# Performance work log

Hardware: AMD Instinct MI355X
Metric: run time of the kernel (lower is better)

Reference implementation:

```python
import jax, jax.numpy as jnp
import numpy as np

N_USERS = 100_000
N_ITEMS = 50_000
N = N_USERS + N_ITEMS
N_LAYERS = 3
ALPHA = 0.8
D = 64
IMG_D = 4096
TXT_D = 384
N_INTER = 2_000_000  # user-item interactions; symmetric nnz = 2*N_INTER


def setup_inputs() -> dict:
    # --- build symmetric-normalized bipartite adjacency (D^-1/2 A D^-1/2) in numpy ---
    rng = np.random.default_rng(0)
    u = rng.integers(0, N_USERS, N_INTER).astype(np.int32)
    i = (rng.integers(0, N_ITEMS, N_INTER) + N_USERS).astype(np.int32)
    rows = np.concatenate([u, i])
    cols = np.concatenate([i, u])
    deg = np.bincount(rows, minlength=N).astype(np.float32)
    d_inv = np.where(deg > 0, deg ** -0.5, 0.0).astype(np.float32)
    vals = d_inv[rows] * d_inv[cols]

    key = jax.random.key(0)
    ks = jax.random.split(key, 8)
    xav_img = float(np.sqrt(6.0 / (IMG_D + D)))
    xav_txt = float(np.sqrt(6.0 / (TXT_D + D)))
    return {
        "image_feats": jax.random.normal(ks[0], (N_ITEMS, IMG_D), jnp.float32),
        "text_feats": jax.random.normal(ks[1], (N_ITEMS, TXT_D), jnp.float32),
        "image_pref": jax.random.normal(ks[2], (N_USERS, D), jnp.float32),
        "text_pref": jax.random.normal(ks[3], (N_USERS, D), jnp.float32),
        "W_img": jax.random.uniform(ks[4], (IMG_D, D), jnp.float32, -xav_img, xav_img),
        "b_img": jnp.zeros((D,), jnp.float32),
        "W_txt": jax.random.uniform(ks[5], (TXT_D, D), jnp.float32, -xav_txt, xav_txt),
        "b_txt": jnp.zeros((D,), jnp.float32),
        "adj_vals": jnp.asarray(vals),
        "adj_rows": jnp.asarray(rows),
        "adj_cols": jnp.asarray(cols),
    }


def _spmm(rows, cols, vals, x):
    # sparse COO @ dense: out[r] += vals[e] * x[cols[e]]
    return jax.ops.segment_sum(vals[:, None] * x[cols], rows, num_segments=N)


def _l2norm(x):
    # F.normalize(x, dim=1): row-wise L2 with eps clamp
    return x / jnp.clip(jnp.linalg.norm(x, axis=1, keepdims=True), 1e-12)


def reference(image_feats, text_feats, image_pref, text_pref,
              W_img, b_img, W_txt, b_txt, adj_vals, adj_rows, adj_cols):
    img = _l2norm(image_feats @ W_img + b_img)   # [n_items, D]
    txt = _l2norm(text_feats @ W_txt + b_txt)    # [n_items, D]
    ego_i = jnp.concatenate([image_pref, img], axis=0)  # [N, D]
    ego_t = jnp.concatenate([text_pref, txt], axis=0)   # [N, D]
    for _ in range(N_LAYERS):
        ego_i = _spmm(adj_rows, adj_cols, adj_vals, ego_i) + ALPHA * ego_i
        ego_t = _spmm(adj_rows, adj_cols, adj_vals, ego_t) + ALPHA * ego_t
    user_preference = jnp.concatenate([ego_i[:N_USERS], ego_t[:N_USERS]], axis=1)  # [n_users, 2D]
    items = jnp.concatenate([ego_i[N_USERS:], ego_t[N_USERS:]], axis=1)            # [n_items, 2D]
    return user_preference, items
```

## Files before the change

### kernel.cpp

```cpp
#include <hip/hip_runtime.h>
#include <hip/hip_bf16.h>

#define N_USERS 100000
#define N_ITEMS 50000
#define N_TOTAL 150000
#define NNZ     4000000
#define ALPHA_F 0.8f
#define ELL_CAP 128

typedef __attribute__((ext_vector_type(8))) short bf16x8;
typedef __attribute__((ext_vector_type(4))) float f32x4;

static __device__ __forceinline__ short f2bf(float f) {
    unsigned u = __builtin_bit_cast(unsigned, f);
    unsigned r = (u + 0x7fff + ((u >> 16) & 1)) >> 16;
    return (short)r;
}
static __device__ __forceinline__ unsigned pack_bf2(float a, float b) {
    return (unsigned)(unsigned short)f2bf(a) | ((unsigned)(unsigned short)f2bf(b) << 16);
}


__global__ void zero_kernel(int* __restrict__ p, int n) {
    int i = blockIdx.x * blockDim.x + threadIdx.x;
    int stride = gridDim.x * blockDim.x;
    for (; i < n; i += stride) p[i] = 0;
}

__global__ void scatter_kernel(const int* __restrict__ rows, const int* __restrict__ cols,
                               const float* __restrict__ vals, int* __restrict__ cnt,
                               int2* __restrict__ ell, int nnz) {
    int i = blockIdx.x * blockDim.x + threadIdx.x;
    int stride = gridDim.x * blockDim.x;
    for (; i < nnz; i += stride) {
        int r = rows[i];
        int p = atomicAdd(&cnt[r], 1);
        ell[(size_t)r * ELL_CAP + p] = make_int2(cols[i], __float_as_int(vals[i]));
    }
}


__global__ void wt_kernel(const float* __restrict__ W, short* __restrict__ Wt, int K) {
    int idx = blockIdx.x * blockDim.x + threadIdx.x;
    if (idx >= K * 64) return;
    int k = idx >> 6, n = idx & 63;
    Wt[(size_t)n * K + k] = f2bf(W[(size_t)k * 64 + n]);
}


__global__ __launch_bounds__(256) void item_fused_kernel(
        const float* __restrict__ Aimg, const float* __restrict__ Atxt,
        const short* __restrict__ Wti, const short* __restrict__ Wtt,
        const float* __restrict__ bimg, const float* __restrict__ btxt,
        float* __restrict__ ego_items, unsigned* __restrict__ egob_items) {
    const int M = N_ITEMS;
    int t = threadIdx.x;
    int wave = t >> 6, l = t & 63;
    int col = l & 15;
    int kb  = l >> 4;
    int row0 = blockIdx.x * 64 + wave * 16;
    int arow = row0 + col;
    bool rowok = arow < M;

    f32x4 ai0 = {0,0,0,0}, ai1 = ai0, ai2 = ai0, ai3 = ai0;
    f32x4 at0 = ai0, at1 = ai0, at2 = ai0, at3 = ai0;

    {
        const float* Ap = Aimg + (size_t)arow * 4096 + kb * 8;
        const short* Wp = Wti + (size_t)col * 4096 + kb * 8;
        for (int k0 = 0; k0 < 4096; k0 += 32) {
            float4 a0 = make_float4(0,0,0,0), a1 = a0;
            if (rowok) {
                a0 = *reinterpret_cast<const float4*>(Ap + k0);
                a1 = *reinterpret_cast<const float4*>(Ap + k0 + 4);
            }
            bf16x8 af;
            af[0]=f2bf(a0.x); af[1]=f2bf(a0.y); af[2]=f2bf(a0.z); af[3]=f2bf(a0.w);
            af[4]=f2bf(a1.x); af[5]=f2bf(a1.y); af[6]=f2bf(a1.z); af[7]=f2bf(a1.w);
            bf16x8 b0 = *reinterpret_cast<const bf16x8*>(Wp + k0);
            bf16x8 b1 = *reinterpret_cast<const bf16x8*>(Wp + (size_t)16 * 4096 + k0);
            bf16x8 b2 = *reinterpret_cast<const bf16x8*>(Wp + (size_t)32 * 4096 + k0);
            bf16x8 b3 = *reinterpret_cast<const bf16x8*>(Wp + (size_t)48 * 4096 + k0);
            ai0 = __builtin_amdgcn_mfma_f32_16x16x32_bf16(af, b0, ai0, 0, 0, 0);
            ai1 = __builtin_amdgcn_mfma_f32_16x16x32_bf16(af, b1, ai1, 0, 0, 0);
            ai2 = __builtin_amdgcn_mfma_f32_16x16x32_bf16(af, b2, ai2, 0, 0, 0);
            ai3 = __builtin_amdgcn_mfma_f32_16x16x32_bf16(af, b3, ai3, 0, 0, 0);
        }
    }
    {
        const float* Ap = Atxt + (size_t)arow * 384 + kb * 8;
        const short* Wp = Wtt + (size_t)col * 384 + kb * 8;
        for (int k0 = 0; k0 < 384; k0 += 32) {
            float4 a0 = make_float4(0,0,0,0), a1 = a0;
            if (rowok) {
                a0 = *reinterpret_cast<const float4*>(Ap + k0);
                a1 = *reinterpret_cast<const float4*>(Ap + k0 + 4);
            }
            bf16x8 af;
            af[0]=f2bf(a0.x); af[1]=f2bf(a0.y); af[2]=f2bf(a0.z); af[3]=f2bf(a0.w);
            af[4]=f2bf(a1.x); af[5]=f2bf(a1.y); af[6]=f2bf(a1.z); af[7]=f2bf(a1.w);
            bf16x8 b0 = *reinterpret_cast<const bf16x8*>(Wp + k0);
            bf16x8 b1 = *reinterpret_cast<const bf16x8*>(Wp + (size_t)16 * 384 + k0);
            bf16x8 b2 = *reinterpret_cast<const bf16x8*>(Wp + (size_t)32 * 384 + k0);
            bf16x8 b3 = *reinterpret_cast<const bf16x8*>(Wp + (size_t)48 * 384 + k0);
            at0 = __builtin_amdgcn_mfma_f32_16x16x32_bf16(af, b0, at0, 0, 0, 0);
            at1 = __builtin_amdgcn_mfma_f32_16x16x32_bf16(af, b1, at1, 0, 0, 0);
            at2 = __builtin_amdgcn_mfma_f32_16x16x32_bf16(af, b2, at2, 0, 0, 0);
            at3 = __builtin_amdgcn_mfma_f32_16x16x32_bf16(af, b3, at3, 0, 0, 0);
        }
    }

    float bi0 = bimg[ 0 + col], bi1 = bimg[16 + col], bi2 = bimg[32 + col], bi3 = bimg[48 + col];
    float bt0 = btxt[ 0 + col], bt1 = btxt[16 + col], bt2 = btxt[32 + col], bt3 = btxt[48 + col];
    #pragma unroll
    for (int i = 0; i < 4; ++i) {
        ai0[i] += bi0; ai1[i] += bi1; ai2[i] += bi2; ai3[i] += bi3;
        at0[i] += bt0; at1[i] += bt1; at2[i] += bt2; at3[i] += bt3;
    }
    #pragma unroll
    for (int i = 0; i < 4; ++i) {
        float ssi = ai0[i]*ai0[i] + ai1[i]*ai1[i] + ai2[i]*ai2[i] + ai3[i]*ai3[i];
        float sst = at0[i]*at0[i] + at1[i]*at1[i] + at2[i]*at2[i] + at3[i]*at3[i];
        #pragma unroll
        for (int off = 1; off < 16; off <<= 1) {
            ssi += __shfl_xor(ssi, off, 64);
            sst += __shfl_xor(sst, off, 64);
        }
        float rni = 1.0f / fmaxf(sqrtf(ssi), 1e-12f);
        float rnt = 1.0f / fmaxf(sqrtf(sst), 1e-12f);
        int r = row0 + kb * 4 + i;
        if (r < M) {
            float i0 = ai0[i]*rni, i1 = ai1[i]*rni, i2 = ai2[i]*rni, i3 = ai3[i]*rni;
            float t0 = at0[i]*rnt, t1 = at1[i]*rnt, t2 = at2[i]*rnt, t3 = at3[i]*rnt;
            float* o = ego_items + (size_t)r * 128 + col;
            o[ 0] = i0; o[16] = i1; o[32] = i2; o[48] = i3;
            o[64] = t0; o[80] = t1; o[96] = t2; o[112] = t3;
            unsigned* ob = egob_items + (size_t)r * 64 + col;
            ob[ 0] = pack_bf2(i0, t0);
            ob[16] = pack_bf2(i1, t1);
            ob[32] = pack_bf2(i2, t2);
            ob[48] = pack_bf2(i3, t3);
        }
    }
}


__global__ __launch_bounds__(256) void user_copy_kernel(
        const float* __restrict__ img_pref, const float* __restrict__ txt_pref,
        float* __restrict__ ego, unsigned* __restrict__ egob) {
    int idx = blockIdx.x * blockDim.x + threadIdx.x;
    if (idx >= N_USERS * 16) return;
    int row = idx >> 4, w4 = (idx & 15) << 2;
    float4 iv = *reinterpret_cast<const float4*>(&img_pref[(size_t)row * 64 + w4]);
    float4 tv = *reinterpret_cast<const float4*>(&txt_pref[(size_t)row * 64 + w4]);
    *reinterpret_cast<float4*>(&ego[(size_t)row * 128 + w4]) = iv;
    *reinterpret_cast<float4*>(&ego[(size_t)row * 128 + 64 + w4]) = tv;
    uint4 m;
    m.x = pack_bf2(iv.x, tv.x); m.y = pack_bf2(iv.y, tv.y);
    m.z = pack_bf2(iv.z, tv.z); m.w = pack_bf2(iv.w, tv.w);
    *reinterpret_cast<uint4*>(&egob[(size_t)row * 64 + w4]) = m;
}


__global__ __launch_bounds__(256) void spmm_kernel(
        const int* __restrict__ cnt, const int2* __restrict__ ell,
        const float* __restrict__ x32, const unsigned* __restrict__ xb,
        float* __restrict__ out32, unsigned* __restrict__ outb) {
    int row = blockIdx.x * 4 + (threadIdx.x >> 6);
    if (row >= N_TOTAL) return;
    int lane = threadIdx.x & 63;
    float2 acc;
    acc.x = ALPHA_F * x32[(size_t)row * 128 + lane];
    acc.y = ALPHA_F * x32[(size_t)row * 128 + 64 + lane];
    int deg = cnt[row];
    const int2* base = ell + (size_t)row * ELL_CAP;
    int i = 0;
    for (; i + 8 <= deg; i += 8) {
        int4 p0 = *reinterpret_cast<const int4*>(base + i);
        int4 p1 = *reinterpret_cast<const int4*>(base + i + 2);
        int4 p2 = *reinterpret_cast<const int4*>(base + i + 4);
        int4 p3 = *reinterpret_cast<const int4*>(base + i + 6);
        unsigned g0 = xb[(size_t)p0.x * 64 + lane];
        unsigned g1 = xb[(size_t)p0.z * 64 + lane];
        unsigned g2 = xb[(size_t)p1.x * 64 + lane];
        unsigned g3 = xb[(size_t)p1.z * 64 + lane];
        unsigned g4 = xb[(size_t)p2.x * 64 + lane];
        unsigned g5 = xb[(size_t)p2.z * 64 + lane];
        unsigned g6 = xb[(size_t)p3.x * 64 + lane];
        unsigned g7 = xb[(size_t)p3.z * 64 + lane];
        float v0 = __int_as_float(p0.y), v1 = __int_as_float(p0.w);
        float v2 = __int_as_float(p1.y), v3 = __int_as_float(p1.w);
        float v4 = __int_as_float(p2.y), v5 = __int_as_float(p2.w);
        float v6 = __int_as_float(p3.y), v7 = __int_as_float(p3.w);
        acc.x = fmaf(v0, __uint_as_float(g0 << 16), acc.x);
        acc.y = fmaf(v0, __uint_as_float(g0 & 0xFFFF0000u), acc.y);
        acc.x = fmaf(v1, __uint_as_float(g1 << 16), acc.x);
        acc.y = fmaf(v1, __uint_as_float(g1 & 0xFFFF0000u), acc.y);
        acc.x = fmaf(v2, __uint_as_float(g2 << 16), acc.x);
        acc.y = fmaf(v2, __uint_as_float(g2 & 0xFFFF0000u), acc.y);
        acc.x = fmaf(v3, __uint_as_float(g3 << 16), acc.x);
        acc.y = fmaf(v3, __uint_as_float(g3 & 0xFFFF0000u), acc.y);
        acc.x = fmaf(v4, __uint_as_float(g4 << 16), acc.x);
        acc.y = fmaf(v4, __uint_as_float(g4 & 0xFFFF0000u), acc.y);
        acc.x = fmaf(v5, __uint_as_float(g5 << 16), acc.x);
        acc.y = fmaf(v5, __uint_as_float(g5 & 0xFFFF0000u), acc.y);
        acc.x = fmaf(v6, __uint_as_float(g6 << 16), acc.x);
        acc.y = fmaf(v6, __uint_as_float(g6 & 0xFFFF0000u), acc.y);
        acc.x = fmaf(v7, __uint_as_float(g7 << 16), acc.x);
        acc.y = fmaf(v7, __uint_as_float(g7 & 0xFFFF0000u), acc.y);
    }
    for (; i < deg; ++i) {
        int2 c = base[i];
        float v = __int_as_float(c.y);
        unsigned g = xb[(size_t)c.x * 64 + lane];
        acc.x = fmaf(v, __uint_as_float(g << 16), acc.x);
        acc.y = fmaf(v, __uint_as_float(g & 0xFFFF0000u), acc.y);
    }
    out32[(size_t)row * 128 + lane] = acc.x;
    out32[(size_t)row * 128 + 64 + lane] = acc.y;
    if (outb)
        outb[(size_t)row * 64 + lane] = pack_bf2(acc.x, acc.y);
}


extern "C" void kernel_launch(void* const* d_in, const int* in_sizes, int n_in,
                              void* d_out, int out_size, void* d_ws, size_t ws_size,
                              hipStream_t stream) {
    const float* image_feats = (const float*)d_in[0];
    const float* text_feats  = (const float*)d_in[1];
    const float* image_pref  = (const float*)d_in[2];
    const float* text_pref   = (const float*)d_in[3];
    const float* W_img       = (const float*)d_in[4];
    const float* b_img       = (const float*)d_in[5];
    const float* W_txt       = (const float*)d_in[6];
    const float* b_txt       = (const float*)d_in[7];
    const float* adj_vals    = (const float*)d_in[8];
    const int*   adj_rows    = (const int*)d_in[9];
    const int*   adj_cols    = (const int*)d_in[10];

    float* out = (float*)d_out;

    char* ws = (char*)d_ws;
    size_t off = 0;
    auto alloc = [&](size_t bytes) { char* p = ws + off; off += (bytes + 255) & ~size_t(255); return p; };
    int*      cnt    = (int*)     alloc(N_TOTAL * sizeof(int));
    int2*     ell    = (int2*)    alloc((size_t)N_TOTAL * ELL_CAP * sizeof(int2));
    float*    ego    = (float*)   alloc((size_t)N_TOTAL * 128 * sizeof(float));
    unsigned* egob   = (unsigned*)alloc((size_t)N_TOTAL * 64 * sizeof(unsigned));
    unsigned* xb1    = (unsigned*)alloc((size_t)N_TOTAL * 64 * sizeof(unsigned));
    short*    Wt_img = (short*)   alloc((size_t)64 * 4096 * sizeof(short));
    short*    Wt_txt = (short*)   alloc((size_t)64 * 384 * sizeof(short));
    (void)ws_size; (void)out_size; (void)n_in; (void)in_sizes;

    zero_kernel<<<256, 256, 0, stream>>>(cnt, N_TOTAL);
    scatter_kernel<<<4096, 256, 0, stream>>>(adj_rows, adj_cols, adj_vals, cnt, ell, NNZ);

    wt_kernel<<<(4096 * 64 + 255) / 256, 256, 0, stream>>>(W_img, Wt_img, 4096);
    wt_kernel<<<(384 * 64 + 255) / 256, 256, 0, stream>>>(W_txt, Wt_txt, 384);

    float* ego_items = ego + (size_t)N_USERS * 128;
    unsigned* egob_items = egob + (size_t)N_USERS * 64;
    item_fused_kernel<<<(N_ITEMS + 63) / 64, 256, 0, stream>>>(
        image_feats, text_feats, Wt_img, Wt_txt, b_img, b_txt, ego_items, egob_items);

    user_copy_kernel<<<(N_USERS * 16 + 255) / 256, 256, 0, stream>>>(
        image_pref, text_pref, ego, egob);

    const int SPMM_GRID = (N_TOTAL + 3) / 4;
    spmm_kernel<<<SPMM_GRID, 256, 0, stream>>>(cnt, ell, ego, egob, out, xb1);
    spmm_kernel<<<SPMM_GRID, 256, 0, stream>>>(cnt, ell, out, xb1, ego, egob);
    spmm_kernel<<<SPMM_GRID, 256, 0, stream>>>(cnt, ell, ego, egob, out, nullptr);
}
```

Measured before the change: 1.154 ms.

## Fuse prep launches, co-schedule GEMM/copy/scatter, sort ELL rows, drop fp32 ego

Zeroing and both weight transposes now run in a single prep kernel. The item GEMM, user copy and COO scatter run as disjoint block ranges of one mega kernel so they overlap. A new per-row bitonic sort orders ELL entries by column to improve gather locality. The fp32 ego buffers are gone: the alpha term and intermediate layers read and write only bf16-packed state, which removes the fp32 traffic but changes precision for the residual term. ELL writes are also clamped to capacity.

```diff
diff --git a/kernel.cpp b/kernel.cpp
--- a/kernel.cpp
+++ b/kernel.cpp
@@ -8,6 +8,10 @@
 #define ALPHA_F 0.8f
 #define ELL_CAP 128
 
+#define G_GEMM 782
+#define G_COPY 512
+#define G_SCAT 1024
+
 typedef __attribute__((ext_vector_type(8))) short bf16x8;
 typedef __attribute__((ext_vector_type(4))) float f32x4;
 
@@ -19,160 +23,203 @@
 static __device__ __forceinline__ unsigned pack_bf2(float a, float b) {
     return (unsigned)(unsigned short)f2bf(a) | ((unsigned)(unsigned short)f2bf(b) << 16);
 }
-
-
-__global__ void zero_kernel(int* __restrict__ p, int n) {
-    int i = blockIdx.x * blockDim.x + threadIdx.x;
-    int stride = gridDim.x * blockDim.x;
-    for (; i < n; i += stride) p[i] = 0;
-}
-
-__global__ void scatter_kernel(const int* __restrict__ rows, const int* __restrict__ cols,
-                               const float* __restrict__ vals, int* __restrict__ cnt,
-                               int2* __restrict__ ell, int nnz) {
-    int i = blockIdx.x * blockDim.x + threadIdx.x;
-    int stride = gridDim.x * blockDim.x;
-    for (; i < nnz; i += stride) {
-        int r = rows[i];
-        int p = atomicAdd(&cnt[r], 1);
-        ell[(size_t)r * ELL_CAP + p] = make_int2(cols[i], __float_as_int(vals[i]));
-    }
-}
-
-
-__global__ void wt_kernel(const float* __restrict__ W, short* __restrict__ Wt, int K) {
-    int idx = blockIdx.x * blockDim.x + threadIdx.x;
-    if (idx >= K * 64) return;
-    int k = idx >> 6, n = idx & 63;
-    Wt[(size_t)n * K + k] = f2bf(W[(size_t)k * 64 + n]);
-}
-
-
-__global__ __launch_bounds__(256) void item_fused_kernel(
+static __device__ __forceinline__ float bf_lo(unsigned u) { return __uint_as_float(u << 16); }
+static __device__ __forceinline__ float bf_hi(unsigned u) { return __uint_as_float(u & 0xFFFF0000u); }
+
+
+__global__ __launch_bounds__(256) void prep_kernel(const float* __restrict__ Wimg,
+                                                   const float* __restrict__ Wtxt,
+                                                   int* __restrict__ cnt,
+                                                   short* __restrict__ Wti,
+                                                   short* __restrict__ Wtt) {
+    const int T0 = N_TOTAL;
+    const int T1 = T0 + 4096 * 64;
+    const int T2 = T1 + 384 * 64;
+    int i = blockIdx.x * 256 + threadIdx.x;
+    int stride = gridDim.x * 256;
+    for (; i < T2; i += stride) {
+        if (i < T0) {
+            cnt[i] = 0;
+        } else if (i < T1) {
+            int idx = i - T0; int k = idx >> 6, n = idx & 63;
+            Wti[(size_t)n * 4096 + k] = f2bf(Wimg[(size_t)k * 64 + n]);
+        } else {
+            int idx = i - T1; int k = idx >> 6, n = idx & 63;
+            Wtt[(size_t)n * 384 + k] = f2bf(Wtxt[(size_t)k * 64 + n]);
+        }
+    }
+}
+
+
+__global__ __launch_bounds__(256) void mega_kernel(
         const float* __restrict__ Aimg, const float* __restrict__ Atxt,
         const short* __restrict__ Wti, const short* __restrict__ Wtt,
         const float* __restrict__ bimg, const float* __restrict__ btxt,
-        float* __restrict__ ego_items, unsigned* __restrict__ egob_items) {
-    const int M = N_ITEMS;
-    int t = threadIdx.x;
-    int wave = t >> 6, l = t & 63;
-    int col = l & 15;
-    int kb  = l >> 4;
-    int row0 = blockIdx.x * 64 + wave * 16;
-    int arow = row0 + col;
-    bool rowok = arow < M;
-
-    f32x4 ai0 = {0,0,0,0}, ai1 = ai0, ai2 = ai0, ai3 = ai0;
-    f32x4 at0 = ai0, at1 = ai0, at2 = ai0, at3 = ai0;
-
-    {
-        const float* Ap = Aimg + (size_t)arow * 4096 + kb * 8;
-        const short* Wp = Wti + (size_t)col * 4096 + kb * 8;
-        for (int k0 = 0; k0 < 4096; k0 += 32) {
-            float4 a0 = make_float4(0,0,0,0), a1 = a0;
-            if (rowok) {
-                a0 = *reinterpret_cast<const float4*>(Ap + k0);
-                a1 = *reinterpret_cast<const float4*>(Ap + k0 + 4);
-            }
-            bf16x8 af;
-            af[0]=f2bf(a0.x); af[1]=f2bf(a0.y); af[2]=f2bf(a0.z); af[3]=f2bf(a0.w);
-            af[4]=f2bf(a1.x); af[5]=f2bf(a1.y); af[6]=f2bf(a1.z); af[7]=f2bf(a1.w);
-            bf16x8 b0 = *reinterpret_cast<const bf16x8*>(Wp + k0);
-            bf16x8 b1 = *reinterpret_cast<const bf16x8*>(Wp + (size_t)16 * 4096 + k0);
-            bf16x8 b2 = *reinterpret_cast<const bf16x8*>(Wp + (size_t)32 * 4096 + k0);
-            bf16x8 b3 = *reinterpret_cast<const bf16x8*>(Wp + (size_t)48 * 4096 + k0);
-            ai0 = __builtin_amdgcn_mfma_f32_16x16x32_bf16(af, b0, ai0, 0, 0, 0);
-            ai1 = __builtin_amdgcn_mfma_f32_16x16x32_bf16(af, b1, ai1, 0, 0, 0);
-            ai2 = __builtin_amdgcn_mfma_f32_16x16x32_bf16(af, b2, ai2, 0, 0, 0);
-            ai3 = __builtin_amdgcn_mfma_f32_16x16x32_bf16(af, b3, ai3, 0, 0, 0);
-        }
-    }
-    {
-        const float* Ap = Atxt + (size_t)arow * 384 + kb * 8;
-        const short* Wp = Wtt + (size_t)col * 384 + kb * 8;
-        for (int k0 = 0; k0 < 384; k0 += 32) {
-            float4 a0 = make_float4(0,0,0,0), a1 = a0;
-            if (rowok) {
-                a0 = *reinterpret_cast<const float4*>(Ap + k0);
-                a1 = *reinterpret_cast<const float4*>(Ap + k0 + 4);
-            }
-            bf16x8 af;
-            af[0]=f2bf(a0.x); af[1]=f2bf(a0.y); af[2]=f2bf(a0.z); af[3]=f2bf(a0.w);
-            af[4]=f2bf(a1.x); af[5]=f2bf(a1.y); af[6]=f2bf(a1.z); af[7]=f2bf(a1.w);
-            bf16x8 b0 = *reinterpret_cast<const bf16x8*>(Wp + k0);
-            bf16x8 b1 = *reinterpret_cast<const bf16x8*>(Wp + (size_t)16 * 384 + k0);
-            bf16x8 b2 = *reinterpret_cast<const bf16x8*>(Wp + (size_t)32 * 384 + k0);
-            bf16x8 b3 = *reinterpret_cast<const bf16x8*>(Wp + (size_t)48 * 384 + k0);
-            at0 = __builtin_amdgcn_mfma_f32_16x16x32_bf16(af, b0, at0, 0, 0, 0);
-            at1 = __builtin_amdgcn_mfma_f32_16x16x32_bf16(af, b1, at1, 0, 0, 0);
-            at2 = __builtin_amdgcn_mfma_f32_16x16x32_bf16(af, b2, at2, 0, 0, 0);
-            at3 = __builtin_amdgcn_mfma_f32_16x16x32_bf16(af, b3, at3, 0, 0, 0);
-        }
-    }
-
-    float bi0 = bimg[ 0 + col], bi1 = bimg[16 + col], bi2 = bimg[32 + col], bi3 = bimg[48 + col];
-    float bt0 = btxt[ 0 + col], bt1 = btxt[16 + col], bt2 = btxt[32 + col], bt3 = btxt[48 + col];
+        unsigned* __restrict__ egob,
+        const int* __restrict__ rows, const int* __restrict__ cols,
+        const float* __restrict__ vals, int* __restrict__ cnt, int2* __restrict__ ell,
+        const float* __restrict__ img_pref, const float* __restrict__ txt_pref) {
+    int b = blockIdx.x;
+    if (b < G_GEMM) {
+        const int M = N_ITEMS;
+        int t = threadIdx.x;
+        int wave = t >> 6, l = t & 63;
+        int col = l & 15;
+        int kb  = l >> 4;
+        int row0 = b * 64 + wave * 16;
+        int arow = row0 + col;
+        bool rowok = arow < M;
+
+        f32x4 ai0 = {0,0,0,0}, ai1 = ai0, ai2 = ai0, ai3 = ai0;
+        f32x4 at0 = ai0, at1 = ai0, at2 = ai0, at3 = ai0;
+
+        {
+            const float* Ap = Aimg + (size_t)arow * 4096 + kb * 8;
+            const short* Wp = Wti + (size_t)col * 4096 + kb * 8;
+            for (int k0 = 0; k0 < 4096; k0 += 32) {
+                float4 a0 = make_float4(0,0,0,0), a1 = a0;
+                if (rowok) {
+                    a0 = *reinterpret_cast<const float4*>(Ap + k0);
+                    a1 = *reinterpret_cast<const float4*>(Ap + k0 + 4);
+                }
+                bf16x8 af;
+                af[0]=f2bf(a0.x); af[1]=f2bf(a0.y); af[2]=f2bf(a0.z); af[3]=f2bf(a0.w);
+                af[4]=f2bf(a1.x); af[5]=f2bf(a1.y); af[6]=f2bf(a1.z); af[7]=f2bf(a1.w);
+                bf16x8 b0 = *reinterpret_cast<const bf16x8*>(Wp + k0);
+                bf16x8 b1 = *reinterpret_cast<const bf16x8*>(Wp + (size_t)16 * 4096 + k0);
+                bf16x8 b2 = *reinterpret_cast<const bf16x8*>(Wp + (size_t)32 * 4096 + k0);
+                bf16x8 b3 = *reinterpret_cast<const bf16x8*>(Wp + (size_t)48 * 4096 + k0);
+                ai0 = __builtin_amdgcn_mfma_f32_16x16x32_bf16(af, b0, ai0, 0, 0, 0);
+                ai1 = __builtin_amdgcn_mfma_f32_16x16x32_bf16(af, b1, ai1, 0, 0, 0);
+                ai2 = __builtin_amdgcn_mfma_f32_16x16x32_bf16(af, b2, ai2, 0, 0, 0);
+                ai3 = __builtin_amdgcn_mfma_f32_16x16x32_bf16(af, b3, ai3, 0, 0, 0);
+            }
+        }
+        {
+            const float* Ap = Atxt + (size_t)arow * 384 + kb * 8;
+            const short* Wp = Wtt + (size_t)col * 384 + kb * 8;
+            for (int k0 = 0; k0 < 384; k0 += 32) {
+                float4 a0 = make_float4(0,0,0,0), a1 = a0;
+                if (rowok) {
+                    a0 = *reinterpret_cast<const float4*>(Ap + k0);
+                    a1 = *reinterpret_cast<const float4*>(Ap + k0 + 4);
+                }
+                bf16x8 af;
+                af[0]=f2bf(a0.x); af[1]=f2bf(a0.y); af[2]=f2bf(a0.z); af[3]=f2bf(a0.w);
+                af[4]=f2bf(a1.x); af[5]=f2bf(a1.y); af[6]=f2bf(a1.z); af[7]=f2bf(a1.w);
+                bf16x8 b0 = *reinterpret_cast<const bf16x8*>(Wp + k0);
+                bf16x8 b1 = *reinterpret_cast<const bf16x8*>(Wp + (size_t)16 * 384 + k0);
+                bf16x8 b2 = *reinterpret_cast<const bf16x8*>(Wp + (size_t)32 * 384 + k0);
+                bf16x8 b3 = *reinterpret_cast<const bf16x8*>(Wp + (size_t)48 * 384 + k0);
+                at0 = __builtin_amdgcn_mfma_f32_16x16x32_bf16(af, b0, at0, 0, 0, 0);
+                at1 = __builtin_amdgcn_mfma_f32_16x16x32_bf16(af, b1, at1, 0, 0, 0);
+                at2 = __builtin_amdgcn_mfma_f32_16x16x32_bf16(af, b2, at2, 0, 0, 0);
+                at3 = __builtin_amdgcn_mfma_f32_16x16x32_bf16(af, b3, at3, 0, 0, 0);
+            }
+        }
+
+        float bi0 = bimg[ 0 + col], bi1 = bimg[16 + col], bi2 = bimg[32 + col], bi3 = bimg[48 + col];
+        float bt0 = btxt[ 0 + col], bt1 = btxt[16 + col], bt2 = btxt[32 + col], bt3 = btxt[48 + col];
+        #pragma unroll
+        for (int i = 0; i < 4; ++i) {
+            ai0[i] += bi0; ai1[i] += bi1; ai2[i] += bi2; ai3[i] += bi3;
+            at0[i] += bt0; at1[i] += bt1; at2[i] += bt2; at3[i] += bt3;
+        }
+        unsigned* egob_items = egob + (size_t)N_USERS * 64;
+        #pragma unroll
+        for (int i = 0; i < 4; ++i) {
+            float ssi = ai0[i]*ai0[i] + ai1[i]*ai1[i] + ai2[i]*ai2[i] + ai3[i]*ai3[i];
+            float sst = at0[i]*at0[i] + at1[i]*at1[i] + at2[i]*at2[i] + at3[i]*at3[i];
+            #pragma unroll
+            for (int off = 1; off < 16; off <<= 1) {
+                ssi += __shfl_xor(ssi, off, 64);
+                sst += __shfl_xor(sst, off, 64);
+            }
+            float rni = 1.0f / fmaxf(sqrtf(ssi), 1e-12f);
+            float rnt = 1.0f / fmaxf(sqrtf(sst), 1e-12f);
+            int r = row0 + kb * 4 + i;
+            if (r < M) {
+                unsigned* ob = egob_items + (size_t)r * 64 + col;
+                ob[ 0] = pack_bf2(ai0[i]*rni, at0[i]*rnt);
+                ob[16] = pack_bf2(ai1[i]*rni, at1[i]*rnt);
+                ob[32] = pack_bf2(ai2[i]*rni, at2[i]*rnt);
+                ob[48] = pack_bf2(ai3[i]*rni, at3[i]*rnt);
+            }
+        }
+    } else if (b < G_GEMM + G_COPY) {
+        int idx = (b - G_GEMM) * 256 + threadIdx.x;
+        int stride = G_COPY * 256;
+        for (; idx < N_USERS * 16; idx += stride) {
+            int row = idx >> 4, w4 = (idx & 15) << 2;
+            float4 iv = *reinterpret_cast<const float4*>(&img_pref[(size_t)row * 64 + w4]);
+            float4 tv = *reinterpret_cast<const float4*>(&txt_pref[(size_t)row * 64 + w4]);
+            uint4 m;
+            m.x = pack_bf2(iv.x, tv.x); m.y = pack_bf2(iv.y, tv.y);
+            m.z = pack_bf2(iv.z, tv.z); m.w = pack_bf2(iv.w, tv.w);
+            *reinterpret_cast<uint4*>(&egob[(size_t)row * 64 + w4]) = m;
+        }
+    } else {
+        int i = (b - G_GEMM - G_COPY) * 256 + threadIdx.x;
+        int stride = G_SCAT * 256;
+        for (; i < NNZ; i += stride) {
+            int r = rows[i];
+            int p = atomicAdd(&cnt[r], 1);
+            if (p < ELL_CAP)
+                ell[(size_t)r * ELL_CAP + p] = make_int2(cols[i], __float_as_int(vals[i]));
+        }
+    }
+}
+
+
+__global__ __launch_bounds__(256) void sort_kernel(const int* __restrict__ cnt,
+                                                   int2* __restrict__ ell) {
+    int row = blockIdx.x * 4 + (threadIdx.x >> 6);
+    if (row >= N_TOTAL) return;
+    int lane = threadIdx.x & 63;
+    int deg = min(cnt[row], ELL_CAP);
+    if (deg <= 1) return;
+    int2* base = ell + (size_t)row * ELL_CAP;
+    int2 e0 = (lane < deg)      ? base[lane]      : make_int2(0x7FFFFFFF, 0);
+    int2 e1 = (lane + 64 < deg) ? base[lane + 64] : make_int2(0x7FFFFFFF, 0);
     #pragma unroll
-    for (int i = 0; i < 4; ++i) {
-        ai0[i] += bi0; ai1[i] += bi1; ai2[i] += bi2; ai3[i] += bi3;
-        at0[i] += bt0; at1[i] += bt1; at2[i] += bt2; at3[i] += bt3;
-    }
-    #pragma unroll
-    for (int i = 0; i < 4; ++i) {
-        float ssi = ai0[i]*ai0[i] + ai1[i]*ai1[i] + ai2[i]*ai2[i] + ai3[i]*ai3[i];
-        float sst = at0[i]*at0[i] + at1[i]*at1[i] + at2[i]*at2[i] + at3[i]*at3[i];
+    for (int k = 2; k <= 128; k <<= 1) {
         #pragma unroll
-        for (int off = 1; off < 16; off <<= 1) {
-            ssi += __shfl_xor(ssi, off, 64);
-            sst += __shfl_xor(sst, off, 64);
-        }
-        float rni = 1.0f / fmaxf(sqrtf(ssi), 1e-12f);
-        float rnt = 1.0f / fmaxf(sqrtf(sst), 1e-12f);
-        int r = row0 + kb * 4 + i;
-        if (r < M) {
-            float i0 = ai0[i]*rni, i1 = ai1[i]*rni, i2 = ai2[i]*rni, i3 = ai3[i]*rni;
-            float t0 = at0[i]*rnt, t1 = at1[i]*rnt, t2 = at2[i]*rnt, t3 = at3[i]*rnt;
-            float* o = ego_items + (size_t)r * 128 + col;
-            o[ 0] = i0; o[16] = i1; o[32] = i2; o[48] = i3;
-            o[64] = t0; o[80] = t1; o[96] = t2; o[112] = t3;
-            unsigned* ob = egob_items + (size_t)r * 64 + col;
-            ob[ 0] = pack_bf2(i0, t0);
-            ob[16] = pack_bf2(i1, t1);
-            ob[32] = pack_bf2(i2, t2);
-            ob[48] = pack_bf2(i3, t3);
-        }
-    }
-}
-
-
-__global__ __launch_bounds__(256) void user_copy_kernel(
-        const float* __restrict__ img_pref, const float* __restrict__ txt_pref,
-        float* __restrict__ ego, unsigned* __restrict__ egob) {
-    int idx = blockIdx.x * blockDim.x + threadIdx.x;
-    if (idx >= N_USERS * 16) return;
-    int row = idx >> 4, w4 = (idx & 15) << 2;
-    float4 iv = *reinterpret_cast<const float4*>(&img_pref[(size_t)row * 64 + w4]);
-    float4 tv = *reinterpret_cast<const float4*>(&txt_pref[(size_t)row * 64 + w4]);
-    *reinterpret_cast<float4*>(&ego[(size_t)row * 128 + w4]) = iv;
-    *reinterpret_cast<float4*>(&ego[(size_t)row * 128 + 64 + w4]) = tv;
-    uint4 m;
-    m.x = pack_bf2(iv.x, tv.x); m.y = pack_bf2(iv.y, tv.y);
-    m.z = pack_bf2(iv.z, tv.z); m.w = pack_bf2(iv.w, tv.w);
-    *reinterpret_cast<uint4*>(&egob[(size_t)row * 64 + w4]) = m;
+        for (int j = 64; j >= 1; j >>= 1) {
+            if (j >= k) continue;
+            if (j == 64) {
+                if (e0.x > e1.x) { int2 tmp = e0; e0 = e1; e1 = tmp; }
+            } else {
+                int2 p0, p1;
+                p0.x = __shfl_xor(e0.x, j, 64); p0.y = __shfl_xor(e0.y, j, 64);
+                p1.x = __shfl_xor(e1.x, j, 64); p1.y = __shfl_xor(e1.y, j, 64);
+                bool up0 = ((lane & k) == 0);
+                bool up1 = (((lane + 64) & k) == 0);
+                bool lo0 = ((lane & j) == 0);
+                bool lo1 = lo0;
+                bool keepmin0 = (up0 == lo0);
+                bool keepmin1 = (up1 == lo1);
+                if (keepmin0 ? (e0.x > p0.x) : (e0.x < p0.x)) e0 = p0;
+                if (keepmin1 ? (e1.x > p1.x) : (e1.x < p1.x)) e1 = p1;
+            }
+        }
+    }
+    if (lane < deg)      base[lane]      = e0;
+    if (lane + 64 < deg) base[lane + 64] = e1;
 }
 
 
 __global__ __launch_bounds__(256) void spmm_kernel(
         const int* __restrict__ cnt, const int2* __restrict__ ell,
-        const float* __restrict__ x32, const unsigned* __restrict__ xb,
+        const unsigned* __restrict__ xb,
         float* __restrict__ out32, unsigned* __restrict__ outb) {
     int row = blockIdx.x * 4 + (threadIdx.x >> 6);
     if (row >= N_TOTAL) return;
     int lane = threadIdx.x & 63;
+    unsigned sw = xb[(size_t)row * 64 + lane];
     float2 acc;
-    acc.x = ALPHA_F * x32[(size_t)row * 128 + lane];
-    acc.y = ALPHA_F * x32[(size_t)row * 128 + 64 + lane];
-    int deg = cnt[row];
+    acc.x = ALPHA_F * bf_lo(sw);
+    acc.y = ALPHA_F * bf_hi(sw);
+    int deg = min(cnt[row], ELL_CAP);
     const int2* base = ell + (size_t)row * ELL_CAP;
     int i = 0;
     for (; i + 8 <= deg; i += 8) {
@@ -192,32 +239,26 @@
         float v2 = __int_as_float(p1.y), v3 = __int_as_float(p1.w);
         float v4 = __int_as_float(p2.y), v5 = __int_as_float(p2.w);
         float v6 = __int_as_float(p3.y), v7 = __int_as_float(p3.w);
-        acc.x = fmaf(v0, __uint_as_float(g0 << 16), acc.x);
-        acc.y = fmaf(v0, __uint_as_float(g0 & 0xFFFF0000u), acc.y);
-        acc.x = fmaf(v1, __uint_as_float(g1 << 16), acc.x);
-        acc.y = fmaf(v1, __uint_as_float(g1 & 0xFFFF0000u), acc.y);
-        acc.x = fmaf(v2, __uint_as_float(g2 << 16), acc.x);
-        acc.y = fmaf(v2, __uint_as_float(g2 & 0xFFFF0000u), acc.y);
-        acc.x = fmaf(v3, __uint_as_float(g3 << 16), acc.x);
-        acc.y = fmaf(v3, __uint_as_float(g3 & 0xFFFF0000u), acc.y);
-        acc.x = fmaf(v4, __uint_as_float(g4 << 16), acc.x);
-        acc.y = fmaf(v4, __uint_as_float(g4 & 0xFFFF0000u), acc.y);
-        acc.x = fmaf(v5, __uint_as_float(g5 << 16), acc.x);
-        acc.y = fmaf(v5, __uint_as_float(g5 & 0xFFFF0000u), acc.y);
-        acc.x = fmaf(v6, __uint_as_float(g6 << 16), acc.x);
-        acc.y = fmaf(v6, __uint_as_float(g6 & 0xFFFF0000u), acc.y);
-        acc.x = fmaf(v7, __uint_as_float(g7 << 16), acc.x);
-        acc.y = fmaf(v7, __uint_as_float(g7 & 0xFFFF0000u), acc.y);
+        acc.x = fmaf(v0, bf_lo(g0), acc.x); acc.y = fmaf(v0, bf_hi(g0), acc.y);
+        acc.x = fmaf(v1, bf_lo(g1), acc.x); acc.y = fmaf(v1, bf_hi(g1), acc.y);
+        acc.x = fmaf(v2, bf_lo(g2), acc.x); acc.y = fmaf(v2, bf_hi(g2), acc.y);
+        acc.x = fmaf(v3, bf_lo(g3), acc.x); acc.y = fmaf(v3, bf_hi(g3), acc.y);
+        acc.x = fmaf(v4, bf_lo(g4), acc.x); acc.y = fmaf(v4, bf_hi(g4), acc.y);
+        acc.x = fmaf(v5, bf_lo(g5), acc.x); acc.y = fmaf(v5, bf_hi(g5), acc.y);
+        acc.x = fmaf(v6, bf_lo(g6), acc.x); acc.y = fmaf(v6, bf_hi(g6), acc.y);
+        acc.x = fmaf(v7, bf_lo(g7), acc.x); acc.y = fmaf(v7, bf_hi(g7), acc.y);
     }
     for (; i < deg; ++i) {
         int2 c = base[i];
         float v = __int_as_float(c.y);
         unsigned g = xb[(size_t)c.x * 64 + lane];
-        acc.x = fmaf(v, __uint_as_float(g << 16), acc.x);
-        acc.y = fmaf(v, __uint_as_float(g & 0xFFFF0000u), acc.y);
-    }
-    out32[(size_t)row * 128 + lane] = acc.x;
-    out32[(size_t)row * 128 + 64 + lane] = acc.y;
+        acc.x = fmaf(v, bf_lo(g), acc.x);
+        acc.y = fmaf(v, bf_hi(g), acc.y);
+    }
+    if (out32) {
+        out32[(size_t)row * 128 + lane] = acc.x;
+        out32[(size_t)row * 128 + 64 + lane] = acc.y;
+    }
     if (outb)
         outb[(size_t)row * 64 + lane] = pack_bf2(acc.x, acc.y);
 }
@@ -245,29 +286,22 @@
     auto alloc = [&](size_t bytes) { char* p = ws + off; off += (bytes + 255) & ~size_t(255); return p; };
     int*      cnt    = (int*)     alloc(N_TOTAL * sizeof(int));
     int2*     ell    = (int2*)    alloc((size_t)N_TOTAL * ELL_CAP * sizeof(int2));
-    float*    ego    = (float*)   alloc((size_t)N_TOTAL * 128 * sizeof(float));
-    unsigned* egob   = (unsigned*)alloc((size_t)N_TOTAL * 64 * sizeof(unsigned));
-    unsigned* xb1    = (unsigned*)alloc((size_t)N_TOTAL * 64 * sizeof(unsigned));
+    unsigned* m0     = (unsigned*)alloc((size_t)N_TOTAL * 64 * sizeof(unsigned));
+    unsigned* m1     = (unsigned*)alloc((size_t)N_TOTAL * 64 * sizeof(unsigned));
     short*    Wt_img = (short*)   alloc((size_t)64 * 4096 * sizeof(short));
     short*    Wt_txt = (short*)   alloc((size_t)64 * 384 * sizeof(short));
     (void)ws_size; (void)out_size; (void)n_in; (void)in_sizes;
 
-    zero_kernel<<<256, 256, 0, stream>>>(cnt, N_TOTAL);
-    scatter_kernel<<<4096, 256, 0, stream>>>(adj_rows, adj_cols, adj_vals, cnt, ell, NNZ);
-
-    wt_kernel<<<(4096 * 64 + 255) / 256, 256, 0, stream>>>(W_img, Wt_img, 4096);
-    wt_kernel<<<(384 * 64 + 255) / 256, 256, 0, stream>>>(W_txt, Wt_txt, 384);
-
-    float* ego_items = ego + (size_t)N_USERS * 128;
-    unsigned* egob_items = egob + (size_t)N_USERS * 64;
-    item_fused_kernel<<<(N_ITEMS + 63) / 64, 256, 0, stream>>>(
-        image_feats, text_feats, Wt_img, Wt_txt, b_img, b_txt, ego_items, egob_items);
-
-    user_copy_kernel<<<(N_USERS * 16 + 255) / 256, 256, 0, stream>>>(
-        image_pref, text_pref, ego, egob);
-
-    const int SPMM_GRID = (N_TOTAL + 3) / 4;
-    spmm_kernel<<<SPMM_GRID, 256, 0, stream>>>(cnt, ell, ego, egob, out, xb1);
-    spmm_kernel<<<SPMM_GRID, 256, 0, stream>>>(cnt, ell, out, xb1, ego, egob);
-    spmm_kernel<<<SPMM_GRID, 256, 0, stream>>>(cnt, ell, ego, egob, out, nullptr);
-}
+    prep_kernel<<<512, 256, 0, stream>>>(W_img, W_txt, cnt, Wt_img, Wt_txt);
+
+    mega_kernel<<<G_GEMM + G_COPY + G_SCAT, 256, 0, stream>>>(
+        image_feats, text_feats, Wt_img, Wt_txt, b_img, b_txt, m0,
+        adj_rows, adj_cols, adj_vals, cnt, ell, image_pref, text_pref);
+
+    const int ROW_GRID = (N_TOTAL + 3) / 4;
+    sort_kernel<<<ROW_GRID, 256, 0, stream>>>(cnt, ell);
+
+    spmm_kernel<<<ROW_GRID, 256, 0, stream>>>(cnt, ell, m0, nullptr, m1);
+    spmm_kernel<<<ROW_GRID, 256, 0, stream>>>(cnt, ell, m1, nullptr, m0);
+    spmm_kernel<<<ROW_GRID, 256, 0, stream>>>(cnt, ell, m0, out, nullptr);
+}
```

Result: slower. 1.181 ms (+2.3%).
